# Kernel tuning notes

Measured on AMD Instinct MI355X. Metric: run time of the kernel, lower is better.

Reference implementation:

```python
import jax, jax.numpy as jnp
import numpy as np

DIM = 1024
HEADS = 16
DIM_HEAD = 64
WINDOW = 256  # sliding window size == block size
NEG = -1e9


def rms_norm(x, gamma, size):
    # F.normalize(x, dim=-1) * sqrt(size) * gamma
    nrm = jnp.sqrt(jnp.sum(x * x, axis=-1, keepdims=True))
    return x / jnp.maximum(nrm, 1e-12) * (size ** 0.5) * gamma


def sliding_window_attention(q, k, v, window):
    # q,k,v: [b, h, S, d]; causal local attention: key j valid iff i-window <= j <= i
    b, h, S, d = q.shape
    Bk = window
    nb = S // Bk
    qb = q.reshape(b, h, nb, Bk, d)
    kb = k.reshape(b, h, nb, Bk, d)
    vb = v.reshape(b, h, nb, Bk, d)
    # previous key/value block (zeros for block 0; masked out below)
    k_prev = jnp.pad(kb, ((0, 0), (0, 0), (1, 0), (0, 0), (0, 0)))[:, :, :nb]
    v_prev = jnp.pad(vb, ((0, 0), (0, 0), (1, 0), (0, 0), (0, 0)))[:, :, :nb]
    kctx = jnp.concatenate([k_prev, kb], axis=3)  # [b,h,nb,2Bk,d]
    vctx = jnp.concatenate([v_prev, vb], axis=3)
    scale = 1.0 / jnp.sqrt(jnp.asarray(d, q.dtype))
    scores = jnp.einsum('bhnqd,bhnkd->bhnqk', qb, kctx) * scale  # [b,h,nb,Bk,2Bk]
    qi = jnp.arange(Bk)[:, None]          # local query index
    kj = jnp.arange(2 * Bk)[None, :]      # local key index (offset -Bk rel to block start)
    diff = Bk + qi - kj                   # global i - j
    base = (diff >= 0) & (diff <= window)  # [Bk, 2Bk]
    blk = jnp.arange(nb)[:, None, None]
    key_exists = ((blk - 1) * Bk + kj[None]) >= 0  # [nb,1,2Bk] -> broadcast
    mask = base[None] & key_exists                 # [nb,Bk,2Bk]
    scores = jnp.where(mask[None, None], scores, NEG)
    attn = jax.nn.softmax(scores, axis=-1)
    out = jnp.einsum('bhnqk,bhnkd->bhnqd', attn, vctx)
    return out.reshape(b, h, S, d)


def setup_inputs() -> dict:
    key = jax.random.key(0)
    ks = jax.random.split(key, 6)
    b, S = 2, 4096
    dim_inner = HEADS * DIM_HEAD
    x = jax.random.normal(ks[0], (b, S, DIM), dtype=jnp.float32)
    gamma = jnp.ones((DIM,), dtype=jnp.float32)
    W_qkv = jax.random.normal(ks[1], (DIM, 3 * dim_inner), dtype=jnp.float32) * 0.02
    W_gates = jax.random.normal(ks[2], (DIM, HEADS), dtype=jnp.float32) * 0.02
    b_gates = jnp.zeros((HEADS,), dtype=jnp.float32)
    W_out = jax.random.normal(ks[3], (dim_inner, DIM), dtype=jnp.float32) * 0.02
    return {"x": x, "gamma": gamma, "W_qkv": W_qkv, "W_gates": W_gates,
            "b_gates": b_gates, "W_out": W_out}


def reference(x, gamma, W_qkv, W_gates, b_gates, W_out):
    b, S, dim = x.shape
    xn = rms_norm(x, gamma, dim)
    qkv = xn @ W_qkv                                    # [b,S,3*h*d]
    qkv = qkv.reshape(b, S, 3, HEADS, DIM_HEAD)
    q, k, v = [jnp.transpose(t, (0, 2, 1, 3)) for t in
               (qkv[:, :, 0], qkv[:, :, 1], qkv[:, :, 2])]  # [b,h,S,d]
    out = sliding_window_attention(q, k, v, WINDOW)      # [b,h,S,d]
    gates = xn @ W_gates + b_gates                       # [b,S,h]
    out = out * jax.nn.sigmoid(jnp.transpose(gates, (0, 2, 1)))[..., None]
    out = jnp.transpose(out, (0, 2, 1, 3)).reshape(b, S, HEADS * DIM_HEAD)
    return out @ W_out
```

## Files before the change

kernel.cpp:

```cpp
#include <hip/hip_runtime.h>
#include <hip/hip_bf16.h>
#include <stdint.h>

typedef __bf16 bf16;
typedef __bf16 bf16x4 __attribute__((ext_vector_type(4)));
typedef __bf16 bf16x8 __attribute__((ext_vector_type(8)));
typedef float f32x4 __attribute__((ext_vector_type(4)));

#define GLOBAL_AS __attribute__((address_space(1)))
#define LDS_AS __attribute__((address_space(3)))

__device__ __forceinline__ void g2lds16(const bf16* g, bf16* l) {
  __builtin_amdgcn_global_load_lds((const GLOBAL_AS void*)g, (LDS_AS void*)l, 16, 0, 0);
}

__global__ __launch_bounds__(256) void rmsnorm_kernel(
    const float* __restrict__ x, const float* __restrict__ gamma,
    bf16* __restrict__ xn) {
  __shared__ float wss[4];
  const int t = threadIdx.x;
  const size_t row = blockIdx.x;
  const float* xr = x + row * 1024;

  float4 xv = *(const float4*)&xr[t * 4];
  float v[4] = {xv.x, xv.y, xv.z, xv.w};
  float ss = v[0]*v[0] + v[1]*v[1] + v[2]*v[2] + v[3]*v[3];
#pragma unroll
  for (int mm = 1; mm < 64; mm <<= 1) ss += __shfl_xor(ss, mm);
  if ((t & 63) == 0) wss[t >> 6] = ss;
  __syncthreads();
  ss = wss[0] + wss[1] + wss[2] + wss[3];
  float inv = 32.0f / sqrtf(fmaxf(ss, 1e-24f));

  float4 gv = *(const float4*)&gamma[t * 4];
  float gvv[4] = {gv.x, gv.y, gv.z, gv.w};
  bf16x4 outv;
#pragma unroll
  for (int i = 0; i < 4; ++i) outv[i] = (bf16)(v[i] * inv * gvv[i]);
  *(bf16x4*)&xn[row * 1024 + t * 4] = outv;
}

__global__ void transpose_f32_bf16(const float* __restrict__ in, bf16* __restrict__ out,
                                   int R, int C) {
  __shared__ bf16 tile[32][33];
  const int tx = threadIdx.x, ty = threadIdx.y;
  const int c0 = blockIdx.x * 32, r0 = blockIdx.y * 32;
#pragma unroll
  for (int i = 0; i < 32; i += 8)
    tile[ty + i][tx] = (bf16)in[(size_t)(r0 + ty + i) * C + c0 + tx];
  __syncthreads();
#pragma unroll
  for (int i = 0; i < 32; i += 8)
    out[(size_t)(c0 + ty + i) * R + r0 + tx] = tile[tx][ty + i];
}

__global__ __launch_bounds__(256) void wg_transpose(const float* __restrict__ Wg,
                                                    bf16* __restrict__ BtAug) {
  int idx = blockIdx.x * 256 + threadIdx.x;
  int n = idx >> 10, k = idx & 1023;
  BtAug[(size_t)(3072 + n) * 1024 + k] = (bf16)Wg[(size_t)k * 16 + n];
}

template <typename OutT>
__global__ __launch_bounds__(256) void gemm_bt_128(
    const bf16* __restrict__ A, const bf16* __restrict__ Bt,
    OutT* __restrict__ C, int M, int N, int K) {
  __shared__ bf16 lA[128 * 64];
  __shared__ bf16 lB[128 * 64];
  const int t = threadIdx.x;
  const int w = t >> 6, lane = t & 63;
  const int col0 = lane & 15, quad = lane >> 4;
  const int m0 = blockIdx.y * 128, n0 = blockIdx.x * 128;
  const int wr = (w >> 1) * 64, wc = (w & 1) * 64;

  const int lrow = t >> 3;
  const int sswz = (((t & 7) ^ (lrow & 7)) << 3);

  f32x4 acc[4][4] = {};

  for (int k0 = 0; k0 < K; k0 += 64) {
    __syncthreads();
#pragma unroll
    for (int c = 0; c < 4; ++c) {
      g2lds16(A  + (size_t)(m0 + c * 32 + lrow) * K + k0 + sswz, &lA[c * 2048 + w * 512]);
      g2lds16(Bt + (size_t)(n0 + c * 32 + lrow) * K + k0 + sswz, &lB[c * 2048 + w * 512]);
    }
    __syncthreads();

#pragma unroll
    for (int kh = 0; kh < 2; ++kh) {
      bf16x8 af[4], bfr[4];
#pragma unroll
      for (int i = 0; i < 4; ++i) {
        int row = wr + i * 16 + col0;
        af[i] = *(const bf16x8*)&lA[row * 64 + (((kh * 4 + quad) ^ (row & 7)) << 3)];
      }
#pragma unroll
      for (int j = 0; j < 4; ++j) {
        int row = wc + j * 16 + col0;
        bfr[j] = *(const bf16x8*)&lB[row * 64 + (((kh * 4 + quad) ^ (row & 7)) << 3)];
      }
#pragma unroll
      for (int i = 0; i < 4; ++i)
#pragma unroll
        for (int j = 0; j < 4; ++j)
          acc[i][j] = __builtin_amdgcn_mfma_f32_16x16x32_bf16(af[i], bfr[j], acc[i][j], 0, 0, 0);
    }
  }

#pragma unroll
  for (int i = 0; i < 4; ++i)
#pragma unroll
    for (int j = 0; j < 4; ++j)
#pragma unroll
      for (int r = 0; r < 4; ++r) {
        int row = m0 + wr + i * 16 + quad * 4 + r;
        int col = n0 + wc + j * 16 + col0;
        C[(size_t)row * N + col] = (OutT)acc[i][j][r];
      }
}

template <typename OutT>
__global__ __launch_bounds__(512, 2) void gemm_bt_256(
    const bf16* __restrict__ A, const bf16* __restrict__ Bt,
    OutT* __restrict__ C, int M, int N, int K) {
  extern __shared__ bf16 lds[];
  bf16* A0 = lds;
  bf16* B0 = lds + 16384;
  bf16* A1 = lds + 32768;
  bf16* B1 = lds + 49152;

  const int t = threadIdx.x;
  const int w = t >> 6, lane = t & 63;
  const int wm = w >> 2, wn = w & 3;
  const int col0 = lane & 15, quad = lane >> 4;
  const int s_sub = lane >> 3;
  const int sswz = (((lane & 7) ^ s_sub) << 3);

  int nwg = gridDim.x * gridDim.y;
  int bid = blockIdx.y * gridDim.x + blockIdx.x;
  int swz = bid;
  if ((nwg & 7) == 0) swz = (bid & 7) * (nwg >> 3) + (bid >> 3);
  const int n0 = (swz % gridDim.x) * 256;
  const int m0 = (swz / gridDim.x) * 256;

  const bf16* Abase = A + (size_t)m0 * (size_t)K;

  auto stageA = [&](int ks, int c, bf16* dstA) {
    int rb = (w < 4) ? (c * 32 + w * 8) : (128 + c * 32 + (w - 4) * 8);
    g2lds16(Abase + (size_t)(rb + s_sub) * K + ks + sswz, dstA + rb * 64);
  };
  auto stageB = [&](int ks, int c, bf16* dstB) {
    int rb = c * 64 + w * 8;
    int gr = n0 + rb + s_sub;
    gr = (gr < N) ? gr : (N - 1);
    g2lds16(Bt + (size_t)gr * (size_t)K + ks + sswz, dstB + rb * 64);
  };

  f32x4 acc[8][4] = {};
  const int NT = K >> 6;
  const int NI = NT >> 1;

#pragma unroll
  for (int c = 0; c < 4; ++c) stageB(0, c, B0);
#pragma unroll
  for (int c = 0; c < 4; ++c) stageA(0, c, A0);

  for (int i = 0; i < NI; ++i) {
#pragma unroll
    for (int h = 0; h < 2; ++h) {
      bf16* cA = h ? A1 : A0;
      bf16* cB = h ? B1 : B0;
      bf16* nA = h ? A0 : A1;
      bf16* nB = h ? B0 : B1;
      int tn = 2 * i + h + 1;
      int kn = ((tn < NT) ? tn : 0) << 6;

      asm volatile("s_waitcnt vmcnt(4)" ::: "memory");
      __builtin_amdgcn_s_barrier();

      bf16x8 bv[4][2];
#pragma unroll
      for (int nj = 0; nj < 4; ++nj) {
        int br = wn * 64 + nj * 16 + col0;
#pragma unroll
        for (int ks = 0; ks < 2; ++ks)
          bv[nj][ks] = *(const bf16x8*)&cB[br * 64 + (((ks * 4 + quad) ^ (br & 7)) << 3)];
      }

      stageB(kn, 0, nB); stageB(kn, 1, nB); stageB(kn, 2, nB); stageB(kn, 3, nB);
      stageA(kn, 0, nA); stageA(kn, 1, nA); stageA(kn, 2, nA); stageA(kn, 3, nA);

      asm volatile("s_waitcnt vmcnt(8)" ::: "memory");
      __builtin_amdgcn_s_barrier();

#pragma unroll
      for (int p = 0; p < 4; ++p) {
        bf16x8 af[2][2];
#pragma unroll
        for (int m2 = 0; m2 < 2; ++m2) {
          int ar = wm * 128 + (p * 2 + m2) * 16 + col0;
#pragma unroll
          for (int ks = 0; ks < 2; ++ks)
            af[m2][ks] = *(const bf16x8*)&cA[ar * 64 + (((ks * 4 + quad) ^ (ar & 7)) << 3)];
        }
        __builtin_amdgcn_s_setprio(1);
#pragma unroll
        for (int ks = 0; ks < 2; ++ks)
#pragma unroll
          for (int m2 = 0; m2 < 2; ++m2)
#pragma unroll
            for (int nj = 0; nj < 4; ++nj)
              acc[p * 2 + m2][nj] = __builtin_amdgcn_mfma_f32_16x16x32_bf16(
                  af[m2][ks], bv[nj][ks], acc[p * 2 + m2][nj], 0, 0, 0);
        __builtin_amdgcn_s_setprio(0);
      }
    }
  }
  asm volatile("s_waitcnt vmcnt(0)" ::: "memory");

#pragma unroll
  for (int mi = 0; mi < 8; ++mi)
#pragma unroll
    for (int nj = 0; nj < 4; ++nj) {
      int col = n0 + wn * 64 + nj * 16 + col0;
      if (col < N) {
        size_t base = (size_t)(m0 + wm * 128 + mi * 16 + quad * 4) * N + col;
#pragma unroll
        for (int r = 0; r < 4; ++r)
          C[base + (size_t)r * N] = (OutT)acc[mi][nj][r];
      }
    }
}

#define NEG_BIG -1e30f
__global__ __launch_bounds__(256) void attn_kernel(
    const bf16* __restrict__ qkv, const float* __restrict__ bg,
    bf16* __restrict__ attnO) {
  __shared__ bf16 lQ[64 * 64];
  __shared__ bf16 lKV[320 * 64];
  __shared__ bf16 lP[4 * 16 * 32];

  const int t = threadIdx.x;
  const int w = t >> 6, lane = t & 63;
  const int col0 = lane & 15, quad = lane >> 4;

  const int blk = blockIdx.x;
  const int g = blk & 63;
  const int h = (blk >> 6) & 15;
  const int bb = blk >> 10;
  const int qs = g * 64;

  const size_t rs = 3200;
  const bf16* qbase = qkv + ((size_t)bb * 4096) * rs + h * 64;

  for (int c = t; c < 64 * 8; c += 256) {
    int row = c >> 3, ck = c & 7;
    *(uint4*)&lQ[row * 64 + ((ck ^ (row & 7)) << 3)] =
        *(const uint4*)(qbase + (size_t)(qs + row) * rs + ck * 8);
  }
  for (int c = t; c < 320 * 8; c += 256) {
    int row = c >> 3, ck = c & 7;
    int j = qs - 256 + row;
    uint4 val = {0, 0, 0, 0};
    if (j >= 0) val = *(const uint4*)(qbase + 1024 + (size_t)j * rs + ck * 8);
    *(uint4*)&lKV[row * 64 + ((ck ^ (row & 7)) << 3)] = val;
  }
  __syncthreads();

  const int qrow = w * 16 + col0;
  bf16x8 a0 = *(const bf16x8*)&lQ[qrow * 64 + ((quad ^ (qrow & 7)) << 3)];
  bf16x8 a1 = *(const bf16x8*)&lQ[qrow * 64 + (((4 + quad) ^ (qrow & 7)) << 3)];
  f32x4 s[20];
#pragma unroll
  for (int kt = 0; kt < 20; ++kt) {
    int krow = kt * 16 + col0;
    bf16x8 b0 = *(const bf16x8*)&lKV[krow * 64 + ((quad ^ (krow & 7)) << 3)];
    bf16x8 b1 = *(const bf16x8*)&lKV[krow * 64 + (((4 + quad) ^ (krow & 7)) << 3)];
    f32x4 z = {};
    z = __builtin_amdgcn_mfma_f32_16x16x32_bf16(a0, b0, z, 0, 0, 0);
    z = __builtin_amdgcn_mfma_f32_16x16x32_bf16(a1, b1, z, 0, 0, 0);
    s[kt] = z;
  }
  __syncthreads();

  {
    const int jl = t & 31, dg = t >> 5;
#pragma unroll
    for (int cc = 0; cc < 10; ++cc) {
      int j = qs - 256 + cc * 32 + jl;
      bf16 tmp[8];
      if (j >= 0) {
        *(uint4*)tmp = *(const uint4*)(qbase + 2048 + (size_t)j * rs + dg * 8);
      } else {
#pragma unroll
        for (int d2 = 0; d2 < 8; ++d2) tmp[d2] = (bf16)0.f;
      }
      int ck = cc * 4 + (jl >> 3);
      int wi = jl & 7;
#pragma unroll
      for (int d2 = 0; d2 < 8; ++d2) {
        int d = dg * 8 + d2;
        lKV[d * 320 + ((ck ^ (d & 7)) << 3) + wi] = tmp[d2];
      }
    }
  }

  float mrow[4] = {NEG_BIG, NEG_BIG, NEG_BIG, NEG_BIG};
  float lrow[4] = {0, 0, 0, 0};
#pragma unroll
  for (int kt = 0; kt < 20; ++kt) {
    int c = kt * 16 + col0;
#pragma unroll
    for (int r = 0; r < 4; ++r) {
      int ql = w * 16 + quad * 4 + r;
      bool valid = (c >= ql) && (c <= ql + 256) && (qs - 256 + c >= 0);
      float sv = valid ? s[kt][r] * 0.125f : NEG_BIG;
      s[kt][r] = sv;
      mrow[r] = fmaxf(mrow[r], sv);
    }
  }
#pragma unroll
  for (int mm = 1; mm < 16; mm <<= 1)
#pragma unroll
    for (int r = 0; r < 4; ++r) mrow[r] = fmaxf(mrow[r], __shfl_xor(mrow[r], mm));
#pragma unroll
  for (int kt = 0; kt < 20; ++kt)
#pragma unroll
    for (int r = 0; r < 4; ++r) {
      float p = __expf(s[kt][r] - mrow[r]);
      s[kt][r] = p;
      lrow[r] += p;
    }
#pragma unroll
  for (int mm = 1; mm < 16; mm <<= 1)
#pragma unroll
    for (int r = 0; r < 4; ++r) lrow[r] += __shfl_xor(lrow[r], mm);

  __syncthreads();

  f32x4 o[4] = {};
  bf16* pw = &lP[w * 512];
#pragma unroll
  for (int kc = 0; kc < 10; ++kc) {
#pragma unroll
    for (int r = 0; r < 4; ++r) {
      pw[(quad * 4 + r) * 32 + col0]      = (bf16)s[2 * kc][r];
      pw[(quad * 4 + r) * 32 + 16 + col0] = (bf16)s[2 * kc + 1][r];
    }
    asm volatile("s_waitcnt lgkmcnt(0)" ::: "memory");
    bf16x8 pa = *(const bf16x8*)&pw[col0 * 32 + quad * 8];
#pragma unroll
    for (int n = 0; n < 4; ++n) {
      int d = n * 16 + col0;
      bf16x8 bvv = *(const bf16x8*)&lKV[d * 320 + (((kc * 4 + quad) ^ (d & 7)) << 3)];
      o[n] = __builtin_amdgcn_mfma_f32_16x16x32_bf16(pa, bvv, o[n], 0, 0, 0);
    }
  }

  const bf16* gbase = qkv + ((size_t)bb * 4096) * rs + 3072 + h;
  const float bgh = bg[h];
#pragma unroll
  for (int r = 0; r < 4; ++r) {
    int ql = w * 16 + quad * 4 + r;
    int srow = qs + ql;
    float logit = (float)gbase[(size_t)srow * rs] + bgh;
    float gate = 1.f / (1.f + __expf(-logit));
    float scale = gate / lrow[r];
#pragma unroll
    for (int n = 0; n < 4; ++n)
      attnO[((size_t)bb * 4096 + srow) * 1024 + h * 64 + n * 16 + col0] =
          (bf16)(o[n][r] * scale);
  }
}

extern "C" void kernel_launch(void* const* d_in, const int* in_sizes, int n_in,
                              void* d_out, int out_size, void* d_ws, size_t ws_size,
                              hipStream_t stream) {
  const float *x = nullptr, *gamma = nullptr, *Wqkv = nullptr,
              *Wg = nullptr, *bg = nullptr, *Wout = nullptr;
  for (int i = 0; i < n_in; ++i) {
    switch (in_sizes[i]) {
      case 8388608: x     = (const float*)d_in[i]; break;
      case 1024:    gamma = (const float*)d_in[i]; break;
      case 3145728: Wqkv  = (const float*)d_in[i]; break;
      case 16384:   Wg    = (const float*)d_in[i]; break;
      case 16:      bg    = (const float*)d_in[i]; break;
      case 1048576: Wout  = (const float*)d_in[i]; break;
    }
  }
  float* out = (float*)d_out;

  static bool attr_done = false;
  if (!attr_done) {
    hipFuncSetAttribute(reinterpret_cast<const void*>(&gemm_bt_256<bf16>),
                        hipFuncAttributeMaxDynamicSharedMemorySize, 131072);
    attr_done = true;
  }

  char* ws = (char*)d_ws;
  bf16* qkv   = (bf16*)ws;  ws += (size_t)8192 * 3200 * 2;
  bf16* xn    = (bf16*)ws;
  bf16* attnO = (bf16*)ws;  ws += (size_t)8192 * 1024 * 2;
  bf16* BtAug = (bf16*)ws;  ws += (size_t)3200 * 1024 * 2;
  bf16* WoutT = (bf16*)ws;  ws += (size_t)1024 * 1024 * 2;

  hipMemsetAsync(BtAug + (size_t)3088 * 1024, 0, (size_t)112 * 1024 * 2, stream);

  rmsnorm_kernel<<<8192, 256, 0, stream>>>(x, gamma, xn);
  transpose_f32_bf16<<<dim3(3072 / 32, 1024 / 32), dim3(32, 8), 0, stream>>>(Wqkv, BtAug, 1024, 3072);
  wg_transpose<<<64, 256, 0, stream>>>(Wg, BtAug);
  transpose_f32_bf16<<<dim3(1024 / 32, 1024 / 32), dim3(32, 8), 0, stream>>>(Wout, WoutT, 1024, 1024);
  gemm_bt_256<bf16><<<dim3(13, 32), 512, 131072, stream>>>(xn, BtAug, qkv, 8192, 3200, 1024);
  attn_kernel<<<2048, 256, 0, stream>>>(qkv, bg, attnO);
  gemm_bt_128<float><<<dim3(1024 / 128, 8192 / 128), 256, 0, stream>>>(attnO, WoutT, out, 8192, 1024, 1024);
}
```

Baseline: 258.1 us.

## Interleave global-to-LDS staging with MFMA sub-steps in 256x256 GEMM

Restructures the 256x256 bf16 GEMM main loop so each K-tile is split into four quarter-steps. Each quarter issues two of the next tile's global-to-LDS loads, waits on a tuned vmcnt, and runs its MFMA batch, rather than issuing all eight loads at once before compute. Staging now maps rows by thread id with a simpler swizzle, and the per-wave M tiling is reorganised to 4x2 sub-tiles. The aim is to spread memory traffic across compute and shorten the stalls at each barrier. The cost is more barriers per tile and tighter dependence on the wait counts being correct.

Result: no change. 257.5 us (-0.2%).

```diff
diff --git a/kernel.cpp b/kernel.cpp
--- a/kernel.cpp
+++ b/kernel.cpp
@@ -134,8 +134,7 @@
   const int w = t >> 6, lane = t & 63;
   const int wm = w >> 2, wn = w & 3;
   const int col0 = lane & 15, quad = lane >> 4;
-  const int s_sub = lane >> 3;
-  const int sswz = (((lane & 7) ^ s_sub) << 3);
+  const int sswz = (((t & 7) ^ ((t >> 3) & 7)) << 3);
 
   int nwg = gridDim.x * gridDim.y;
   int bid = blockIdx.y * gridDim.x + blockIdx.x;
@@ -147,90 +146,92 @@
   const bf16* Abase = A + (size_t)m0 * (size_t)K;
 
   auto stageA = [&](int ks, int c, bf16* dstA) {
-    int rb = (w < 4) ? (c * 32 + w * 8) : (128 + c * 32 + (w - 4) * 8);
-    g2lds16(Abase + (size_t)(rb + s_sub) * K + ks + sswz, dstA + rb * 64);
+    int row = c * 64 + (t >> 3);
+    g2lds16(Abase + (size_t)row * K + ks + sswz, dstA + c * 4096 + w * 512);
   };
   auto stageB = [&](int ks, int c, bf16* dstB) {
-    int rb = c * 64 + w * 8;
-    int gr = n0 + rb + s_sub;
+    int gr = n0 + c * 64 + (t >> 3);
     gr = (gr < N) ? gr : (N - 1);
-    g2lds16(Bt + (size_t)gr * (size_t)K + ks + sswz, dstB + rb * 64);
+    g2lds16(Bt + (size_t)gr * (size_t)K + ks + sswz, dstB + c * 4096 + w * 512);
   };
 
-  f32x4 acc[8][4] = {};
+  f32x4 acc[4][2][4] = {};
   const int NT = K >> 6;
-  const int NI = NT >> 1;
-
-#pragma unroll
-  for (int c = 0; c < 4; ++c) stageB(0, c, B0);
-#pragma unroll
-  for (int c = 0; c < 4; ++c) stageA(0, c, A0);
-
-  for (int i = 0; i < NI; ++i) {
-#pragma unroll
-    for (int h = 0; h < 2; ++h) {
-      bf16* cA = h ? A1 : A0;
-      bf16* cB = h ? B1 : B0;
-      bf16* nA = h ? A0 : A1;
-      bf16* nB = h ? B0 : B1;
-      int tn = 2 * i + h + 1;
-      int kn = ((tn < NT) ? tn : 0) << 6;
-
-      asm volatile("s_waitcnt vmcnt(4)" ::: "memory");
+
+  stageB(0, 0, B0); stageB(0, 1, B0); stageB(0, 2, B0); stageB(0, 3, B0);
+  stageA(0, 0, A0);
+  stageA(0, 1, A0); stageA(0, 2, A0); stageA(0, 3, A0);
+  asm volatile("s_waitcnt vmcnt(3)" ::: "memory");
+  __builtin_amdgcn_s_barrier();
+
+  for (int T = 0; T < NT; ++T) {
+    bf16* cA = (T & 1) ? A1 : A0;
+    bf16* cB = (T & 1) ? B1 : B0;
+    bf16* nA = (T & 1) ? A0 : A1;
+    bf16* nB = (T & 1) ? B0 : B1;
+    int tn = T + 1;
+    int kn = ((tn < NT) ? tn : 0) << 6;
+
+    bf16x8 bv[4][2];
+#pragma unroll
+    for (int q = 0; q < 4; ++q) {
+      if (q == 0) {
+#pragma unroll
+        for (int nj = 0; nj < 4; ++nj) {
+          int br = wn * 64 + nj * 16 + col0;
+#pragma unroll
+          for (int ks = 0; ks < 2; ++ks)
+            bv[nj][ks] = *(const bf16x8*)&cB[br * 64 + (((ks * 4 + quad) ^ (br & 7)) << 3)];
+        }
+      }
+      bf16x8 af[2][2];
+#pragma unroll
+      for (int m2 = 0; m2 < 2; ++m2) {
+        int ar = q * 64 + wm * 32 + m2 * 16 + col0;
+#pragma unroll
+        for (int ks = 0; ks < 2; ++ks)
+          af[m2][ks] = *(const bf16x8*)&cA[ar * 64 + (((ks * 4 + quad) ^ (ar & 7)) << 3)];
+      }
+      if (q == 0)      { stageA(kn, 0, nA); stageB(kn, 0, nB); }
+      else if (q == 1) { stageB(kn, 1, nB); stageB(kn, 2, nB); }
+      else if (q == 2) { stageB(kn, 3, nB); stageA(kn, 1, nA); }
+      else             { stageA(kn, 2, nA); stageA(kn, 3, nA); }
+      if (q == 0)      asm volatile("s_waitcnt vmcnt(4)" ::: "memory");
+      else if (q == 1) asm volatile("s_waitcnt vmcnt(5)" ::: "memory");
+      else if (q == 2) asm volatile("s_waitcnt vmcnt(6)" ::: "memory");
+      else             asm volatile("s_waitcnt vmcnt(3)" ::: "memory");
       __builtin_amdgcn_s_barrier();
-
-      bf16x8 bv[4][2];
+      asm volatile("s_waitcnt lgkmcnt(0)" ::: "memory");
+      __builtin_amdgcn_sched_barrier(0);
+      __builtin_amdgcn_s_setprio(1);
+#pragma unroll
+      for (int ks = 0; ks < 2; ++ks)
+#pragma unroll
+        for (int m2 = 0; m2 < 2; ++m2)
+#pragma unroll
+          for (int nj = 0; nj < 4; ++nj)
+            acc[q][m2][nj] = __builtin_amdgcn_mfma_f32_16x16x32_bf16(
+                af[m2][ks], bv[nj][ks], acc[q][m2][nj], 0, 0, 0);
+      __builtin_amdgcn_s_setprio(0);
+      __builtin_amdgcn_s_barrier();
+    }
+  }
+  asm volatile("s_waitcnt vmcnt(0)" ::: "memory");
+
+#pragma unroll
+  for (int q = 0; q < 4; ++q)
+#pragma unroll
+    for (int m2 = 0; m2 < 2; ++m2)
 #pragma unroll
       for (int nj = 0; nj < 4; ++nj) {
-        int br = wn * 64 + nj * 16 + col0;
-#pragma unroll
-        for (int ks = 0; ks < 2; ++ks)
-          bv[nj][ks] = *(const bf16x8*)&cB[br * 64 + (((ks * 4 + quad) ^ (br & 7)) << 3)];
-      }
-
-      stageB(kn, 0, nB); stageB(kn, 1, nB); stageB(kn, 2, nB); stageB(kn, 3, nB);
-      stageA(kn, 0, nA); stageA(kn, 1, nA); stageA(kn, 2, nA); stageA(kn, 3, nA);
-
-      asm volatile("s_waitcnt vmcnt(8)" ::: "memory");
-      __builtin_amdgcn_s_barrier();
-
-#pragma unroll
-      for (int p = 0; p < 4; ++p) {
-        bf16x8 af[2][2];
-#pragma unroll
-        for (int m2 = 0; m2 < 2; ++m2) {
-          int ar = wm * 128 + (p * 2 + m2) * 16 + col0;
-#pragma unroll
-          for (int ks = 0; ks < 2; ++ks)
-            af[m2][ks] = *(const bf16x8*)&cA[ar * 64 + (((ks * 4 + quad) ^ (ar & 7)) << 3)];
+        int col = n0 + wn * 64 + nj * 16 + col0;
+        if (col < N) {
+          size_t base = (size_t)(m0 + q * 64 + wm * 32 + m2 * 16 + quad * 4) * N + col;
+#pragma unroll
+          for (int r = 0; r < 4; ++r)
+            C[base + (size_t)r * N] = (OutT)acc[q][m2][nj][r];
         }
-        __builtin_amdgcn_s_setprio(1);
-#pragma unroll
-        for (int ks = 0; ks < 2; ++ks)
-#pragma unroll
-          for (int m2 = 0; m2 < 2; ++m2)
-#pragma unroll
-            for (int nj = 0; nj < 4; ++nj)
-              acc[p * 2 + m2][nj] = __builtin_amdgcn_mfma_f32_16x16x32_bf16(
-                  af[m2][ks], bv[nj][ks], acc[p * 2 + m2][nj], 0, 0, 0);
-        __builtin_amdgcn_s_setprio(0);
-      }
-    }
-  }
-  asm volatile("s_waitcnt vmcnt(0)" ::: "memory");
-
-#pragma unroll
-  for (int mi = 0; mi < 8; ++mi)
-#pragma unroll
-    for (int nj = 0; nj < 4; ++nj) {
-      int col = n0 + wn * 64 + nj * 16 + col0;
-      if (col < N) {
-        size_t base = (size_t)(m0 + wm * 128 + mi * 16 + quad * 4) * N + col;
-#pragma unroll
-        for (int r = 0; r < 4; ++r)
-          C[base + (size_t)r * N] = (OutT)acc[mi][nj][r];
-      }
-    }
+      }
 }
 
 #define NEG_BIG -1e30f
```
